# Performance work log

Hardware: AMD Instinct MI355X
Metric: run time of the kernel (lower is better)

The kernel has to match this reference:

```python
import jax, jax.numpy as jnp
from jax import lax
import numpy as np

B, T, C = 4, 2048, 1024
H = 4                      # num_heads
D = C // H                 # head_dim
EPS_N = 1e-6               # normalizer eps in scan
EPS_GN = 1e-5              # GroupNorm eps (torch default)


def setup_inputs() -> dict:
    key = jax.random.key(0)
    ks = jax.random.split(key, 8)
    s = 0.02
    return {
        "x": jax.random.normal(ks[0], (B, T, C), jnp.float32),
        "conv_w": jax.random.normal(ks[1], (C, 1, 4), jnp.float32) * s,
        "conv_b": jax.random.normal(ks[2], (C,), jnp.float32) * s,
        "wx_w": jax.random.normal(ks[3], (4 * C, C), jnp.float32) * s,
        "wx_b": jax.random.normal(ks[4], (4 * C,), jnp.float32) * s,
        "gn_w": jnp.ones((C,), jnp.float32),
        "gn_b": jnp.zeros((C,), jnp.float32),
        "out_w": jax.random.normal(ks[5], (C, C), jnp.float32) * s,
        "out_b": jax.random.normal(ks[6], (C,), jnp.float32) * s,
    }


def _slstm_scan(i_g, f_g, z_g, o_g):
    # all inputs (B,T,H,D); scan over time
    def step(carry, g):
        c, n, m = carry
        i_t, f_t, z_t, o_t = g
        m_t = jnp.maximum(f_t + m, i_t)
        i_p = jnp.exp(i_t - m_t)
        f_p = jnp.exp(f_t + m - m_t)
        c_t = f_p * c + i_p * z_t
        n_t = f_p * n + i_p
        h_t = jax.nn.sigmoid(o_t) * (c_t / (n_t + EPS_N))
        return (c_t, n_t, m_t), h_t

    tfirst = lambda a: jnp.transpose(a, (1, 0, 2, 3))  # (T,B,H,D)
    init = (jnp.zeros((B, H, D), i_g.dtype),
            jnp.ones((B, H, D), i_g.dtype),
            jnp.zeros((B, H, D), i_g.dtype))
    _, h_seq = lax.scan(step, init, (tfirst(i_g), tfirst(f_g), tfirst(z_g), tfirst(o_g)))
    return jnp.transpose(h_seq, (1, 0, 2, 3))  # (B,T,H,D)


def reference(x, conv_w, conv_b, wx_w, wx_b, gn_w, gn_b, out_w, out_b):
    # causal depthwise conv (torch pad=3 both sides, sliced to first T == left pad 3)
    xc = jnp.transpose(x, (0, 2, 1))  # (B,C,T)
    xc = lax.conv_general_dilated(
        xc, conv_w, window_strides=(1,), padding=[(3, 0)],
        dimension_numbers=("NCH", "OIH", "NCH"), feature_group_count=C)
    xc = jax.nn.silu(xc + conv_b[None, :, None])
    xc = jnp.transpose(xc, (0, 2, 1))  # (B,T,C)

    gates = jnp.einsum("btc,gc->btg", xc, wx_w) + wx_b  # (B,T,4C)
    gates = gates.reshape(B, T, 4, H, D)
    i_g, f_g, z_g, o_g = (gates[:, :, k] for k in range(4))
    z_g = jnp.tanh(z_g)

    h = _slstm_scan(i_g, f_g, z_g, o_g).reshape(B, T, C)

    # GroupNorm(H groups) over (B,C,T): normalize per (batch, group) over (D, T)
    hg = h.reshape(B, T, H, D)
    mean = hg.mean(axis=(1, 3), keepdims=True)
    var = hg.var(axis=(1, 3), keepdims=True)
    hn = ((hg - mean) / jnp.sqrt(var + EPS_GN)).reshape(B, T, C)
    hn = hn * gn_w + gn_b

    out = jnp.einsum("btc,oc->bto", hn, out_w) + out_b
    return out + x  # dropout is identity at inference
```

## Files before the change

kernel.cpp:

```cpp
#include <hip/hip_runtime.h>

#define B_ 4
#define T_ 2048
#define C_ 1024
#define H_ 4
#define D_ 256
#define M_ (B_*T_)
#define N1_ (4*C_)
#define K_ C_
#define LANES_ (B_*C_)
#define CHUNK_ 32
#define NCHUNK_ (T_/CHUNK_)

typedef unsigned short u16;
typedef unsigned int u32;
typedef __bf16 bf16x8 __attribute__((ext_vector_type(8)));
typedef float f32x4 __attribute__((ext_vector_type(4)));
typedef float vf4 __attribute__((ext_vector_type(4)));
typedef unsigned short u16x4 __attribute__((ext_vector_type(4)));
typedef unsigned short u16x8 __attribute__((ext_vector_type(8)));

__device__ __forceinline__ u16 f2bf(float f) {
  union { float f; u32 u; } v; v.f = f;
  u32 u = v.u;
  u32 r = (u + 0x7FFFu + ((u >> 16) & 1u)) >> 16;
  return (u16)r;
}
__device__ __forceinline__ float b2f(u16 h) {
  union { u32 u; float f; } v; v.u = ((u32)h) << 16;
  return v.f;
}

__global__ void cast_bf16(const float* __restrict__ in, u16* __restrict__ out) {
  int i8 = (blockIdx.x * 256 + threadIdx.x) * 8;
  vf4 a = *(const vf4*)(in + i8);
  vf4 b = *(const vf4*)(in + i8 + 4);
  u16x8 o;
  o[0] = f2bf(a[0]); o[1] = f2bf(a[1]); o[2] = f2bf(a[2]); o[3] = f2bf(a[3]);
  o[4] = f2bf(b[0]); o[5] = f2bf(b[1]); o[6] = f2bf(b[2]); o[7] = f2bf(b[3]);
  *(u16x8*)(out + i8) = o;
}

__global__ void conv_silu(const float* __restrict__ x, const float* __restrict__ cw,
                          const float* __restrict__ cb, u16* __restrict__ xc,
                          float* __restrict__ stats) {
  if (blockIdx.x == 0 && threadIdx.x < 32) stats[threadIdx.x] = 0.f;
  int i4 = (blockIdx.x * 256 + threadIdx.x) * 4;
  int c = i4 & (C_ - 1);
  int t = (i4 >> 10) & (T_ - 1);
  vf4 acc = *(const vf4*)(cb + c);
  vf4 w0 = *(const vf4*)(cw + (size_t)c * 4);
  vf4 w1 = *(const vf4*)(cw + (size_t)(c + 1) * 4);
  vf4 w2 = *(const vf4*)(cw + (size_t)(c + 2) * 4);
  vf4 w3 = *(const vf4*)(cw + (size_t)(c + 3) * 4);
#pragma unroll
  for (int k = 0; k < 4; ++k) {
    if (t - 3 + k >= 0) {
      vf4 xv = *(const vf4*)(x + (size_t)i4 + (size_t)(k - 3) * C_);
      acc[0] = fmaf(w0[k], xv[0], acc[0]);
      acc[1] = fmaf(w1[k], xv[1], acc[1]);
      acc[2] = fmaf(w2[k], xv[2], acc[2]);
      acc[3] = fmaf(w3[k], xv[3], acc[3]);
    }
  }
  u16x4 o;
#pragma unroll
  for (int j = 0; j < 4; ++j) {
    float s = acc[j] / (1.f + __expf(-acc[j]));
    o[j] = f2bf(s);
  }
  *(u16x4*)(xc + i4) = o;
}

template <int EPI>
__global__ __launch_bounds__(256, 2)
void gemm_bt(const u16* __restrict__ A, const u16* __restrict__ Bw,
             const float* __restrict__ bias, const float* __restrict__ resid,
             u16* __restrict__ obf, float* __restrict__ of32,
             int M, int N, int K)
{
  __shared__ __align__(16) u16 a_s[128 * 64];
  __shared__ __align__(16) u16 b_s[128 * 64];

  const int tid  = threadIdx.x;
  const int lane = tid & 63;
  const int l15  = lane & 15;
  const int q    = lane >> 4;
  const int wave = tid >> 6;
  const int wm   = (wave >> 1) * 64;
  const int wn   = (wave & 1) * 64;
  const int bm   = blockIdx.y * 128;
  const int bn   = blockIdx.x * 128;

  const int srow   = wave * 8 + (lane >> 3);
  const int schunk = lane & 7;

  f32x4 acc[4][4];
#pragma unroll
  for (int i = 0; i < 4; ++i)
#pragma unroll
    for (int j = 0; j < 4; ++j) acc[i][j] = (f32x4){0.f, 0.f, 0.f, 0.f};

  for (int k0 = 0; k0 < K; k0 += 64) {
#pragma unroll
    for (int i = 0; i < 4; ++i) {
      int r = i * 32 + srow;
      int lc = schunk ^ (r & 7);
      const u16* ga = A  + (size_t)(bm + r) * K + k0 + lc * 8;
      const u16* gb = Bw + (size_t)(bn + r) * K + k0 + lc * 8;
      __builtin_amdgcn_global_load_lds(
          (const __attribute__((address_space(1))) u32*)ga,
          (__attribute__((address_space(3))) u32*)&a_s[(i * 32 + wave * 8) * 64],
          16, 0, 0);
      __builtin_amdgcn_global_load_lds(
          (const __attribute__((address_space(1))) u32*)gb,
          (__attribute__((address_space(3))) u32*)&b_s[(i * 32 + wave * 8) * 64],
          16, 0, 0);
    }
    __syncthreads();
#pragma unroll
    for (int kk = 0; kk < 64; kk += 32) {
      const int kc = kk >> 3;
      bf16x8 af[4], bfr[4];
#pragma unroll
      for (int s = 0; s < 4; ++s) {
        int ra = wm + s * 16 + l15;
        int ph = (kc + q) ^ (ra & 7);
        af[s] = *(const bf16x8*)&a_s[ra * 64 + ph * 8];
      }
#pragma unroll
      for (int s = 0; s < 4; ++s) {
        int rb = wn + s * 16 + l15;
        int ph = (kc + q) ^ (rb & 7);
        bfr[s] = *(const bf16x8*)&b_s[rb * 64 + ph * 8];
      }
#pragma unroll
      for (int sm = 0; sm < 4; ++sm)
#pragma unroll
        for (int sn = 0; sn < 4; ++sn)
          acc[sm][sn] = __builtin_amdgcn_mfma_f32_16x16x32_bf16(af[sm], bfr[sn], acc[sm][sn], 0, 0, 0);
    }
    __syncthreads();
  }

#pragma unroll
  for (int sm = 0; sm < 4; ++sm) {
#pragma unroll
    for (int r = 0; r < 4; ++r) {
      int row = bm + wm + sm * 16 + q * 4 + r;
#pragma unroll
      for (int sn = 0; sn < 4; ++sn) {
        int col = bn + wn + sn * 16 + l15;
        float v = acc[sm][sn][r] + bias[col];
        if (EPI == 0) {
          if ((col >> 10) == 2) {
            float e = __expf(2.f * v);
            v = (e - 1.f) / (e + 1.f);
          }
          obf[(size_t)row * N + col] = f2bf(v);
        } else {
          v += resid[(size_t)row * N + col];
          of32[(size_t)row * N + col] = v;
        }
      }
    }
  }
}

__global__ void scan_passA(const u16* __restrict__ gates,
                           float* __restrict__ sF, float* __restrict__ sM,
                           float* __restrict__ sBc, float* __restrict__ sBn) {
  int tid = blockIdx.x * 256 + threadIdx.x;
  int lp = tid & 2047;
  int s = tid >> 11;
  int b = lp >> 9;
  int c2 = (lp & 511) * 2;
  const u16* g = gates + (size_t)b * T_ * N1_ + (size_t)(s * CHUNK_) * N1_ + c2;
  float F0 = 0.f, M0 = -1e30f, bc0 = 0.f, bn0 = 0.f;
  float F1 = 0.f, M1 = -1e30f, bc1 = 0.f, bn1 = 0.f;
#pragma unroll 4
  for (int t = 0; t < CHUNK_; ++t) {
    const u16* gt = g + (size_t)t * N1_;
    u32 iw = *(const u32*)(gt);
    u32 fw = *(const u32*)(gt + C_);
    u32 zw = *(const u32*)(gt + 2 * C_);
    {
      float i_t = b2f((u16)iw), f_t = b2f((u16)fw), z_t = b2f((u16)zw);
      float Mf = M0 + f_t;
      float Mn = fmaxf(Mf, i_t);
      float ea = __expf(Mf - Mn), eb = __expf(i_t - Mn);
      bc0 = ea * bc0 + eb * z_t; bn0 = ea * bn0 + eb; F0 += f_t; M0 = Mn;
    }
    {
      float i_t = b2f((u16)(iw >> 16)), f_t = b2f((u16)(fw >> 16)), z_t = b2f((u16)(zw >> 16));
      float Mf = M1 + f_t;
      float Mn = fmaxf(Mf, i_t);
      float ea = __expf(Mf - Mn), eb = __expf(i_t - Mn);
      bc1 = ea * bc1 + eb * z_t; bn1 = ea * bn1 + eb; F1 += f_t; M1 = Mn;
    }
  }
  int idx = s * LANES_ + b * C_ + c2;
  sF[idx] = F0; sM[idx] = M0; sBc[idx] = bc0; sBn[idx] = bn0;
  sF[idx + 1] = F1; sM[idx + 1] = M1; sBc[idx + 1] = bc1; sBn[idx + 1] = bn1;
}

__global__ void scan_prefix(const float* __restrict__ sF, const float* __restrict__ sM,
                            const float* __restrict__ sBc, const float* __restrict__ sBn,
                            float* __restrict__ iC, float* __restrict__ iN,
                            float* __restrict__ iM) {
  int l = blockIdx.x * 256 + threadIdx.x;
  float ct = 0.f, nt = 1.f, mt = 0.f;
  for (int s = 0; s < NCHUNK_; ++s) {
    int idx = s * LANES_ + l;
    iC[idx] = ct; iN[idx] = nt; iM[idx] = mt;
    float F = sF[idx], M = sM[idx], bc = sBc[idx], bn = sBn[idx];
    float mf = mt + F;
    float mn = fmaxf(mf, M);
    float a = __expf(mf - mn);
    float bcoef = __expf(M - mn);
    ct = a * ct + bcoef * bc;
    nt = a * nt + bcoef * bn;
    mt = mn;
  }
}

__global__ void scan_passB(const u16* __restrict__ gates,
                           const float* __restrict__ iC, const float* __restrict__ iN,
                           const float* __restrict__ iM, u16* __restrict__ h,
                           float* __restrict__ stats) {
  int tid = blockIdx.x * 256 + threadIdx.x;
  int lp = tid & 2047;
  int s = tid >> 11;
  int b = lp >> 9;
  int c2 = (lp & 511) * 2;
  const u16* g = gates + (size_t)b * T_ * N1_ + (size_t)(s * CHUNK_) * N1_ + c2;
  u16* hp = h + (size_t)b * T_ * C_ + (size_t)(s * CHUNK_) * C_ + c2;
  int idx = s * LANES_ + b * C_ + c2;
  float cc0 = iC[idx], nn0 = iN[idx], mm0 = iM[idx];
  float cc1 = iC[idx + 1], nn1 = iN[idx + 1], mm1 = iM[idx + 1];
  float ls = 0.f, lq = 0.f;
#pragma unroll 4
  for (int t = 0; t < CHUNK_; ++t) {
    const u16* gt = g + (size_t)t * N1_;
    u32 iw = *(const u32*)(gt);
    u32 fw = *(const u32*)(gt + C_);
    u32 zw = *(const u32*)(gt + 2 * C_);
    u32 ow = *(const u32*)(gt + 3 * C_);
    float h0, h1;
    {
      float i_t = b2f((u16)iw), f_t = b2f((u16)fw), z_t = b2f((u16)zw), o_t = b2f((u16)ow);
      float m_new = fmaxf(f_t + mm0, i_t);
      float i_p = __expf(i_t - m_new);
      float f_p = __expf(f_t + mm0 - m_new);
      cc0 = f_p * cc0 + i_p * z_t;
      nn0 = f_p * nn0 + i_p;
      mm0 = m_new;
      float sig_o = 1.f / (1.f + __expf(-o_t));
      h0 = sig_o * (cc0 / (nn0 + 1e-6f));
    }
    {
      float i_t = b2f((u16)(iw >> 16)), f_t = b2f((u16)(fw >> 16));
      float z_t = b2f((u16)(zw >> 16)), o_t = b2f((u16)(ow >> 16));
      float m_new = fmaxf(f_t + mm1, i_t);
      float i_p = __expf(i_t - m_new);
      float f_p = __expf(f_t + mm1 - m_new);
      cc1 = f_p * cc1 + i_p * z_t;
      nn1 = f_p * nn1 + i_p;
      mm1 = m_new;
      float sig_o = 1.f / (1.f + __expf(-o_t));
      h1 = sig_o * (cc1 / (nn1 + 1e-6f));
    }
    u16 hb0 = f2bf(h0), hb1 = f2bf(h1);
    float v0 = b2f(hb0), v1 = b2f(hb1);
    ls += v0 + v1; lq += v0 * v0 + v1 * v1;
    *(u32*)(hp + (size_t)t * C_) = (u32)hb0 | ((u32)hb1 << 16);
  }
  __shared__ float rs[256], rq[256];
  int thr = threadIdx.x;
  rs[thr] = ls; rq[thr] = lq;
  __syncthreads();
  for (int off = 64; off > 0; off >>= 1) {
    if ((thr & 127) < off) { rs[thr] += rs[thr + off]; rq[thr] += rq[thr + off]; }
    __syncthreads();
  }
  if ((thr & 127) == 0) {
    int grp = b * 4 + (c2 >> 8);
    atomicAdd(&stats[grp * 2 + 0], rs[thr]);
    atomicAdd(&stats[grp * 2 + 1], rq[thr]);
  }
}

__global__ void norm_kernel(const u16* __restrict__ h, const float* __restrict__ stats,
                            const float* __restrict__ gn_w, const float* __restrict__ gn_b,
                            u16* __restrict__ hn) {
  int i8 = (blockIdx.x * 256 + threadIdx.x) * 8;
  int c = i8 & (C_ - 1);
  int b = i8 >> 21;
  int grp = b * 4 + (c >> 8);
  const float inv_n = 1.f / (float)(T_ * D_);
  float mean = stats[grp * 2 + 0] * inv_n;
  float var  = stats[grp * 2 + 1] * inv_n - mean * mean;
  float rstd = rsqrtf(var + 1e-5f);
  u16x8 hv = *(const u16x8*)(h + i8);
  vf4 w0 = *(const vf4*)(gn_w + c), w1 = *(const vf4*)(gn_w + c + 4);
  vf4 b0 = *(const vf4*)(gn_b + c), b1 = *(const vf4*)(gn_b + c + 4);
  u16x8 o;
#pragma unroll
  for (int j = 0; j < 4; ++j) {
    o[j]     = f2bf((b2f(hv[j])     - mean) * rstd * w0[j] + b0[j]);
    o[j + 4] = f2bf((b2f(hv[j + 4]) - mean) * rstd * w1[j] + b1[j]);
  }
  *(u16x8*)(hn + i8) = o;
}

extern "C" void kernel_launch(void* const* d_in, const int* in_sizes, int n_in,
                              void* d_out, int out_size, void* d_ws, size_t ws_size,
                              hipStream_t stream) {
  const float* x      = (const float*)d_in[0];
  const float* conv_w = (const float*)d_in[1];
  const float* conv_b = (const float*)d_in[2];
  const float* wx_w   = (const float*)d_in[3];
  const float* wx_b   = (const float*)d_in[4];
  const float* gn_w   = (const float*)d_in[5];
  const float* gn_b   = (const float*)d_in[6];
  const float* out_w  = (const float*)d_in[7];
  const float* out_b  = (const float*)d_in[8];
  float* out = (float*)d_out;

  char* p = (char*)d_ws;
  u16* xc    = (u16*)p; p += (size_t)M_ * K_ * 2;
  u16* w1    = (u16*)p; p += (size_t)N1_ * K_ * 2;
  u16* w2    = (u16*)p; p += (size_t)C_ * C_ * 2;
  u16* gts   = (u16*)p; p += (size_t)M_ * N1_ * 2;
  u16* hb    = (u16*)p; p += (size_t)M_ * C_ * 2;
  u16* hn    = (u16*)p; p += (size_t)M_ * C_ * 2;
  float* stats = (float*)p; p += 256;
  const int nsum = LANES_ * NCHUNK_;
  float* sF  = (float*)p; p += (size_t)nsum * 4;
  float* sM  = (float*)p; p += (size_t)nsum * 4;
  float* sBc = (float*)p; p += (size_t)nsum * 4;
  float* sBn = (float*)p; p += (size_t)nsum * 4;
  float* iC  = (float*)p; p += (size_t)nsum * 4;
  float* iN  = (float*)p; p += (size_t)nsum * 4;
  float* iM  = (float*)p; p += (size_t)nsum * 4;

  cast_bf16<<<(N1_ * K_) / 2048, 256, 0, stream>>>(wx_w, w1);
  cast_bf16<<<(C_ * C_) / 2048, 256, 0, stream>>>(out_w, w2);

  conv_silu<<<(M_ * C_) / 1024, 256, 0, stream>>>(x, conv_w, conv_b, xc, stats);

  gemm_bt<0><<<dim3(N1_ / 128, M_ / 128), 256, 0, stream>>>(
      xc, w1, wx_b, nullptr, gts, nullptr, M_, N1_, K_);

  scan_passA<<<(2048 * NCHUNK_) / 256, 256, 0, stream>>>(gts, sF, sM, sBc, sBn);
  scan_prefix<<<LANES_ / 256, 256, 0, stream>>>(sF, sM, sBc, sBn, iC, iN, iM);
  scan_passB<<<(2048 * NCHUNK_) / 256, 256, 0, stream>>>(gts, iC, iN, iM, hb, stats);

  norm_kernel<<<(M_ * C_) / 2048, 256, 0, stream>>>(hb, stats, gn_w, gn_b, hn);

  gemm_bt<1><<<dim3(C_ / 128, M_ / 128), 256, 0, stream>>>(
      hn, w2, out_b, x, nullptr, out, M_, C_, K_);
}
```

Baseline: 287.5 us.

## Interleave gate weights and fuse scan pass A into the gate GEMM epilogue

Permutes the gate weight rows so each channel's i,f,z,o gates sit next to each other in the GEMM output. The GEMM epilogue stages its tile in shared memory and computes the per-chunk scan summaries there, which removes the separate pass-A kernel and its re-read of the gate tensor. Pass B now reads all four gates for two channels in one vector load, and the summary and prefix arrays are packed as float4. The two weight casts are merged into one launch. The costs are a larger shared-memory footprint and extra epilogue work in the big GEMM, where only 128 threads run the serial chunk scan.

```diff
diff --git a/kernel.cpp b/kernel.cpp
--- a/kernel.cpp
+++ b/kernel.cpp
@@ -31,14 +31,26 @@
   return v.f;
 }
 
-__global__ void cast_bf16(const float* __restrict__ in, u16* __restrict__ out) {
+__global__ void cast_weights(const float* __restrict__ wx_w, const float* __restrict__ out_w,
+                             u16* __restrict__ w1p, u16* __restrict__ w2) {
   int i8 = (blockIdx.x * 256 + threadIdx.x) * 8;
-  vf4 a = *(const vf4*)(in + i8);
-  vf4 b = *(const vf4*)(in + i8 + 4);
   u16x8 o;
-  o[0] = f2bf(a[0]); o[1] = f2bf(a[1]); o[2] = f2bf(a[2]); o[3] = f2bf(a[3]);
-  o[4] = f2bf(b[0]); o[5] = f2bf(b[1]); o[6] = f2bf(b[2]); o[7] = f2bf(b[3]);
-  *(u16x8*)(out + i8) = o;
+  if (i8 < N1_ * K_) {
+    int n = i8 >> 10, k8 = i8 & 1023;
+    const float* src = wx_w + (size_t)(((n & 3) << 10) | (n >> 2)) * K_ + k8;
+    vf4 a = *(const vf4*)src;
+    vf4 b = *(const vf4*)(src + 4);
+#pragma unroll
+    for (int j = 0; j < 4; ++j) { o[j] = f2bf(a[j]); o[j + 4] = f2bf(b[j]); }
+    *(u16x8*)(w1p + i8) = o;
+  } else {
+    int j8 = i8 - N1_ * K_;
+    vf4 a = *(const vf4*)(out_w + j8);
+    vf4 b = *(const vf4*)(out_w + j8 + 4);
+#pragma unroll
+    for (int j = 0; j < 4; ++j) { o[j] = f2bf(a[j]); o[j + 4] = f2bf(b[j]); }
+    *(u16x8*)(w2 + j8) = o;
+  }
 }
 
 __global__ void conv_silu(const float* __restrict__ x, const float* __restrict__ cw,
@@ -77,10 +89,11 @@
 void gemm_bt(const u16* __restrict__ A, const u16* __restrict__ Bw,
              const float* __restrict__ bias, const float* __restrict__ resid,
              u16* __restrict__ obf, float* __restrict__ of32,
-             int M, int N, int K)
+             f32x4* __restrict__ sSum, int M, int N, int K)
 {
-  __shared__ __align__(16) u16 a_s[128 * 64];
-  __shared__ __align__(16) u16 b_s[128 * 64];
+  __shared__ __align__(16) u16 smem[128 * 132];
+  u16* a_s = smem;
+  u16* b_s = smem + 128 * 64;
 
   const int tid  = threadIdx.x;
   const int lane = tid & 63;
@@ -143,23 +156,58 @@
     __syncthreads();
   }
 
-#pragma unroll
-  for (int sm = 0; sm < 4; ++sm) {
-#pragma unroll
-    for (int r = 0; r < 4; ++r) {
-      int row = bm + wm + sm * 16 + q * 4 + r;
-#pragma unroll
-      for (int sn = 0; sn < 4; ++sn) {
-        int col = bn + wn + sn * 16 + l15;
-        float v = acc[sm][sn][r] + bias[col];
-        if (EPI == 0) {
-          if ((col >> 10) == 2) {
+  if (EPI == 0) {
+#pragma unroll
+    for (int smi = 0; smi < 4; ++smi) {
+#pragma unroll
+      for (int r = 0; r < 4; ++r) {
+        int lrow = wm + smi * 16 + q * 4 + r;
+#pragma unroll
+        for (int sni = 0; sni < 4; ++sni) {
+          int lcol = wn + sni * 16 + l15;
+          int gcol = bn + lcol;
+          float v = acc[smi][sni][r] + bias[((gcol & 3) << 10) | (gcol >> 2)];
+          if ((l15 & 3) == 2) {
             float e = __expf(2.f * v);
             v = (e - 1.f) / (e + 1.f);
           }
-          obf[(size_t)row * N + col] = f2bf(v);
-        } else {
-          v += resid[(size_t)row * N + col];
+          u16 hv = f2bf(v);
+          obf[(size_t)(bm + lrow) * N + gcol] = hv;
+          smem[lrow * 132 + lcol] = hv;
+        }
+      }
+    }
+    __syncthreads();
+    if (tid < 128) {
+      int ch = tid & 31, ck = tid >> 5;
+      const u16* sp = smem + (ck * 32) * 132 + ch * 4;
+      float F = 0.f, Mx = -1e30f, aBc = 0.f, aBn = 0.f;
+#pragma unroll 8
+      for (int t = 0; t < CHUNK_; ++t) {
+        u16x4 gv = *(const u16x4*)(sp + t * 132);
+        float i_t = b2f(gv[0]), f_t = b2f(gv[1]), z_t = b2f(gv[2]);
+        float Mf = Mx + f_t;
+        float Mn = fmaxf(Mf, i_t);
+        float ea = __expf(Mf - Mn), eb = __expf(i_t - Mn);
+        aBc = ea * aBc + eb * z_t;
+        aBn = ea * aBn + eb;
+        F += f_t; Mx = Mn;
+      }
+      int b = bm >> 11;
+      int s = ((bm & 2047) >> 5) + ck;
+      int cg = (bn >> 2) + ch;
+      sSum[(size_t)s * LANES_ + b * C_ + cg] = (f32x4){F, Mx, aBc, aBn};
+    }
+  } else {
+#pragma unroll
+    for (int smi = 0; smi < 4; ++smi) {
+#pragma unroll
+      for (int r = 0; r < 4; ++r) {
+        int row = bm + wm + smi * 16 + q * 4 + r;
+#pragma unroll
+        for (int sni = 0; sni < 4; ++sni) {
+          int col = bn + wn + sni * 16 + l15;
+          float v = acc[smi][sni][r] + bias[col] + resid[(size_t)row * N + col];
           of32[(size_t)row * N + col] = v;
         }
       }
@@ -167,88 +215,44 @@
   }
 }
 
-__global__ void scan_passA(const u16* __restrict__ gates,
-                           float* __restrict__ sF, float* __restrict__ sM,
-                           float* __restrict__ sBc, float* __restrict__ sBn) {
+__global__ void scan_prefix(const f32x4* __restrict__ sSum, f32x4* __restrict__ iSt) {
+  int l = blockIdx.x * 256 + threadIdx.x;
+  float ct = 0.f, nt = 1.f, mt = 0.f;
+#pragma unroll 4
+  for (int s = 0; s < NCHUNK_; ++s) {
+    int idx = s * LANES_ + l;
+    f32x4 S = sSum[idx];
+    iSt[idx] = (f32x4){ct, nt, mt, 0.f};
+    float mf = mt + S[0];
+    float mn = fmaxf(mf, S[1]);
+    float a = __expf(mf - mn);
+    float bcoef = __expf(S[1] - mn);
+    ct = a * ct + bcoef * S[2];
+    nt = a * nt + bcoef * S[3];
+    mt = mn;
+  }
+}
+
+__global__ void scan_passB(const u16* __restrict__ gates, const f32x4* __restrict__ iSt,
+                           u16* __restrict__ h, float* __restrict__ stats) {
   int tid = blockIdx.x * 256 + threadIdx.x;
   int lp = tid & 2047;
   int s = tid >> 11;
   int b = lp >> 9;
   int c2 = (lp & 511) * 2;
-  const u16* g = gates + (size_t)b * T_ * N1_ + (size_t)(s * CHUNK_) * N1_ + c2;
-  float F0 = 0.f, M0 = -1e30f, bc0 = 0.f, bn0 = 0.f;
-  float F1 = 0.f, M1 = -1e30f, bc1 = 0.f, bn1 = 0.f;
-#pragma unroll 4
-  for (int t = 0; t < CHUNK_; ++t) {
-    const u16* gt = g + (size_t)t * N1_;
-    u32 iw = *(const u32*)(gt);
-    u32 fw = *(const u32*)(gt + C_);
-    u32 zw = *(const u32*)(gt + 2 * C_);
-    {
-      float i_t = b2f((u16)iw), f_t = b2f((u16)fw), z_t = b2f((u16)zw);
-      float Mf = M0 + f_t;
-      float Mn = fmaxf(Mf, i_t);
-      float ea = __expf(Mf - Mn), eb = __expf(i_t - Mn);
-      bc0 = ea * bc0 + eb * z_t; bn0 = ea * bn0 + eb; F0 += f_t; M0 = Mn;
-    }
-    {
-      float i_t = b2f((u16)(iw >> 16)), f_t = b2f((u16)(fw >> 16)), z_t = b2f((u16)(zw >> 16));
-      float Mf = M1 + f_t;
-      float Mn = fmaxf(Mf, i_t);
-      float ea = __expf(Mf - Mn), eb = __expf(i_t - Mn);
-      bc1 = ea * bc1 + eb * z_t; bn1 = ea * bn1 + eb; F1 += f_t; M1 = Mn;
-    }
-  }
+  const u16* g = gates + ((size_t)(b * T_ + s * CHUNK_) * C_ + c2) * 4;
+  u16* hp = h + (size_t)(b * T_ + s * CHUNK_) * C_ + c2;
   int idx = s * LANES_ + b * C_ + c2;
-  sF[idx] = F0; sM[idx] = M0; sBc[idx] = bc0; sBn[idx] = bn0;
-  sF[idx + 1] = F1; sM[idx + 1] = M1; sBc[idx + 1] = bc1; sBn[idx + 1] = bn1;
-}
-
-__global__ void scan_prefix(const float* __restrict__ sF, const float* __restrict__ sM,
-                            const float* __restrict__ sBc, const float* __restrict__ sBn,
-                            float* __restrict__ iC, float* __restrict__ iN,
-                            float* __restrict__ iM) {
-  int l = blockIdx.x * 256 + threadIdx.x;
-  float ct = 0.f, nt = 1.f, mt = 0.f;
-  for (int s = 0; s < NCHUNK_; ++s) {
-    int idx = s * LANES_ + l;
-    iC[idx] = ct; iN[idx] = nt; iM[idx] = mt;
-    float F = sF[idx], M = sM[idx], bc = sBc[idx], bn = sBn[idx];
-    float mf = mt + F;
-    float mn = fmaxf(mf, M);
-    float a = __expf(mf - mn);
-    float bcoef = __expf(M - mn);
-    ct = a * ct + bcoef * bc;
-    nt = a * nt + bcoef * bn;
-    mt = mn;
-  }
-}
-
-__global__ void scan_passB(const u16* __restrict__ gates,
-                           const float* __restrict__ iC, const float* __restrict__ iN,
-                           const float* __restrict__ iM, u16* __restrict__ h,
-                           float* __restrict__ stats) {
-  int tid = blockIdx.x * 256 + threadIdx.x;
-  int lp = tid & 2047;
-  int s = tid >> 11;
-  int b = lp >> 9;
-  int c2 = (lp & 511) * 2;
-  const u16* g = gates + (size_t)b * T_ * N1_ + (size_t)(s * CHUNK_) * N1_ + c2;
-  u16* hp = h + (size_t)b * T_ * C_ + (size_t)(s * CHUNK_) * C_ + c2;
-  int idx = s * LANES_ + b * C_ + c2;
-  float cc0 = iC[idx], nn0 = iN[idx], mm0 = iM[idx];
-  float cc1 = iC[idx + 1], nn1 = iN[idx + 1], mm1 = iM[idx + 1];
+  f32x4 S0 = iSt[idx], S1 = iSt[idx + 1];
+  float cc0 = S0[0], nn0 = S0[1], mm0 = S0[2];
+  float cc1 = S1[0], nn1 = S1[1], mm1 = S1[2];
   float ls = 0.f, lq = 0.f;
 #pragma unroll 4
   for (int t = 0; t < CHUNK_; ++t) {
-    const u16* gt = g + (size_t)t * N1_;
-    u32 iw = *(const u32*)(gt);
-    u32 fw = *(const u32*)(gt + C_);
-    u32 zw = *(const u32*)(gt + 2 * C_);
-    u32 ow = *(const u32*)(gt + 3 * C_);
+    u16x8 gv = *(const u16x8*)(g + (size_t)t * C_ * 4);
     float h0, h1;
     {
-      float i_t = b2f((u16)iw), f_t = b2f((u16)fw), z_t = b2f((u16)zw), o_t = b2f((u16)ow);
+      float i_t = b2f(gv[0]), f_t = b2f(gv[1]), z_t = b2f(gv[2]), o_t = b2f(gv[3]);
       float m_new = fmaxf(f_t + mm0, i_t);
       float i_p = __expf(i_t - m_new);
       float f_p = __expf(f_t + mm0 - m_new);
@@ -259,8 +263,7 @@
       h0 = sig_o * (cc0 / (nn0 + 1e-6f));
     }
     {
-      float i_t = b2f((u16)(iw >> 16)), f_t = b2f((u16)(fw >> 16));
-      float z_t = b2f((u16)(zw >> 16)), o_t = b2f((u16)(ow >> 16));
+      float i_t = b2f(gv[4]), f_t = b2f(gv[5]), z_t = b2f(gv[6]), o_t = b2f(gv[7]);
       float m_new = fmaxf(f_t + mm1, i_t);
       float i_p = __expf(i_t - m_new);
       float f_p = __expf(f_t + mm1 - m_new);
@@ -336,28 +339,21 @@
   u16* hn    = (u16*)p; p += (size_t)M_ * C_ * 2;
   float* stats = (float*)p; p += 256;
   const int nsum = LANES_ * NCHUNK_;
-  float* sF  = (float*)p; p += (size_t)nsum * 4;
-  float* sM  = (float*)p; p += (size_t)nsum * 4;
-  float* sBc = (float*)p; p += (size_t)nsum * 4;
-  float* sBn = (float*)p; p += (size_t)nsum * 4;
-  float* iC  = (float*)p; p += (size_t)nsum * 4;
-  float* iN  = (float*)p; p += (size_t)nsum * 4;
-  float* iM  = (float*)p; p += (size_t)nsum * 4;
-
-  cast_bf16<<<(N1_ * K_) / 2048, 256, 0, stream>>>(wx_w, w1);
-  cast_bf16<<<(C_ * C_) / 2048, 256, 0, stream>>>(out_w, w2);
+  f32x4* sSum = (f32x4*)p; p += (size_t)nsum * 16;
+  f32x4* iSt  = (f32x4*)p; p += (size_t)nsum * 16;
+
+  cast_weights<<<(N1_ * K_ + C_ * C_) / 2048, 256, 0, stream>>>(wx_w, out_w, w1, w2);
 
   conv_silu<<<(M_ * C_) / 1024, 256, 0, stream>>>(x, conv_w, conv_b, xc, stats);
 
   gemm_bt<0><<<dim3(N1_ / 128, M_ / 128), 256, 0, stream>>>(
-      xc, w1, wx_b, nullptr, gts, nullptr, M_, N1_, K_);
-
-  scan_passA<<<(2048 * NCHUNK_) / 256, 256, 0, stream>>>(gts, sF, sM, sBc, sBn);
-  scan_prefix<<<LANES_ / 256, 256, 0, stream>>>(sF, sM, sBc, sBn, iC, iN, iM);
-  scan_passB<<<(2048 * NCHUNK_) / 256, 256, 0, stream>>>(gts, iC, iN, iM, hb, stats);
+      xc, w1, wx_b, nullptr, gts, nullptr, sSum, M_, N1_, K_);
+
+  scan_prefix<<<LANES_ / 256, 256, 0, stream>>>(sSum, iSt);
+  scan_passB<<<(2048 * NCHUNK_) / 256, 256, 0, stream>>>(gts, iSt, hb, stats);
 
   norm_kernel<<<(M_ * C_) / 2048, 256, 0, stream>>>(hb, stats, gn_w, gn_b, hn);
 
   gemm_bt<1><<<dim3(C_ / 128, M_ / 128), 256, 0, stream>>>(
-      hn, w2, out_b, x, nullptr, out, M_, C_, K_);
-}
+      hn, w2, out_b, x, nullptr, out, nullptr, M_, C_, K_);
+}
```

Result: no change. 282.3 us (-1.8%).
